# Kernel optimization log

Measured on AMD Instinct MI355X. Metric: run time of the kernel, lower is better.

Reference implementation:

```python
import jax, jax.numpy as jnp
import numpy as np

N = 8192
E = 262144
EMBED = 128
EDGE_DIM = 16
EPS = 1e-09
SLOPE = 0.01  # LeakyReLU default


def leaky_relu(x):
    return jnp.where(x >= 0, x, SLOPE * x)


def setup_inputs() -> dict:
    key = jax.random.key(0)
    ks = jax.random.split(key, 12)
    x = jax.random.randint(ks[0], (N, 1), 0, 20, dtype=jnp.int64)
    edge_index = jax.random.randint(ks[1], (2, E), 0, N, dtype=jnp.int64)
    edge_attr = jax.random.normal(ks[2], (E, EDGE_DIM), dtype=jnp.float32)
    emb = jax.random.normal(ks[3], (20, EMBED), dtype=jnp.float32)
    # conv1: nn = Linear(EMBED, 64); edge lin: EDGE_DIM -> EMBED
    W1 = jax.random.normal(ks[4], (EMBED, 64), dtype=jnp.float32) * 0.05
    b1 = jnp.zeros((64,), dtype=jnp.float32)
    E1w = jax.random.normal(ks[5], (EDGE_DIM, EMBED), dtype=jnp.float32) * 0.1
    E1b = jnp.zeros((EMBED,), dtype=jnp.float32)
    # conv6: nn = Linear(64, 32); edge lin: EDGE_DIM -> 64
    W2 = jax.random.normal(ks[6], (64, 32), dtype=jnp.float32) * 0.05
    b2 = jnp.zeros((32,), dtype=jnp.float32)
    E2w = jax.random.normal(ks[7], (EDGE_DIM, 64), dtype=jnp.float32) * 0.1
    E2b = jnp.zeros((64,), dtype=jnp.float32)
    return {"x": x, "edge_index": edge_index, "edge_attr": edge_attr,
            "emb": emb, "W1": W1, "b1": b1, "E1w": E1w, "E1b": E1b,
            "W2": W2, "b2": b2, "E2w": E2w, "E2b": E2b}


def gine_conv(h, src, dst, edge_emb, W, b):
    # message: relu(h[src] + edge_emb); aggregate: scatter-add at dst
    m = jax.nn.relu(h[src] + edge_emb)                      # [E, d]
    agg = jax.ops.segment_sum(m, dst, num_segments=N)       # [N, d]
    return ((1.0 + EPS) * h + agg) @ W + b


def reference(x, edge_index, edge_attr, emb, W1, b1, E1w, E1b, W2, b2, E2w, E2b):
    h = emb[x[:, 0]]                                         # [N, EMBED]
    src, dst = edge_index[0], edge_index[1]
    h = gine_conv(h, src, dst, edge_attr @ E1w + E1b, W1, b1)  # [N, 64]
    h = leaky_relu(h)
    h = gine_conv(h, src, dst, edge_attr @ E2w + E2b, W2, b2)  # [N, 32]
    return h @ h.T                                           # [N, N]
```

## Files before the change

### kernel.cpp

```cpp
#include <hip/hip_runtime.h>
#include <hip/hip_bf16.h>

#define NN 8192
#define NE 262144
#define EPSF 1e-9f

typedef __attribute__((ext_vector_type(8))) short short8;
typedef __attribute__((ext_vector_type(4))) float floatx4;

__global__ __launch_bounds__(256) void embed_kernel(const int* __restrict__ x,
    const float* __restrict__ emb, float* __restrict__ h0) {
  int tid = blockIdx.x * 256 + threadIdx.x;
  int n = tid >> 5, j = tid & 31;
  int xi = x[n];
  ((float4*)h0)[(size_t)n * 32 + j] = ((const float4*)emb)[xi * 32 + j];
}

__global__ __launch_bounds__(256) void degcount_kernel(const int* __restrict__ ei,
    int* __restrict__ deg) {
  int e = blockIdx.x * 256 + threadIdx.x;
  atomicAdd(&deg[ei[NE + e]], 1);
}

__global__ __launch_bounds__(256) void scan_kernel(const int* __restrict__ deg,
    int* __restrict__ rowptr, int* __restrict__ cursor) {
  __shared__ int part[256];
  int t = threadIdx.x;
  int base = t * 32;
  int local[32];
  int s = 0;
#pragma unroll
  for (int i = 0; i < 32; ++i) { local[i] = deg[base + i]; s += local[i]; }
  part[t] = s;
  __syncthreads();
  int pre = 0;
  for (int i = 0; i < t; ++i) pre += part[i];
  int run = pre;
#pragma unroll
  for (int i = 0; i < 32; ++i) {
    rowptr[base + i] = run;
    cursor[base + i] = run;
    run += local[i];
  }
  if (t == 255) rowptr[NN] = run;
}

__global__ __launch_bounds__(256) void scatter_kernel(const int* __restrict__ ei,
    int* __restrict__ cursor, int2* __restrict__ csr) {
  int e = blockIdx.x * 256 + threadIdx.x;
  int s = ei[e], d = ei[NE + e];
  int pos = atomicAdd(&cursor[d], 1);
  csr[pos] = (int2){e, s};
}

__global__ __launch_bounds__(256) void fused1_kernel(const int* __restrict__ rowptr,
    const int2* __restrict__ csr, const float* __restrict__ ea,
    const float* __restrict__ E1w, const float* __restrict__ E1b,
    const float* __restrict__ W1, const float* __restrict__ b1,
    const float* __restrict__ h0, float* __restrict__ h1) {
  __shared__ float sE[16 * 128];
  __shared__ float sEb[128];
  __shared__ float st[4][128];
  for (int i = threadIdx.x; i < 16 * 128; i += 256) sE[i] = E1w[i];
  if (threadIdx.x < 128) sEb[threadIdx.x] = E1b[threadIdx.x];
  __syncthreads();
  int lane = threadIdx.x & 63;
  int w = threadIdx.x >> 6;
  int n = blockIdx.x * 4 + w;
  int beg = rowptr[n], end = rowptr[n + 1];
  float acc0 = 0.f, acc1 = 0.f;
  int i = beg;
  for (; i + 2 <= end; i += 2) {
    int2 pa = csr[i];
    int2 pb = csr[i + 1];
    int eA = __builtin_amdgcn_readfirstlane(pa.x);
    int sA = __builtin_amdgcn_readfirstlane(pa.y);
    int eB = __builtin_amdgcn_readfirstlane(pb.x);
    int sB = __builtin_amdgcn_readfirstlane(pb.y);
    float hA0 = h0[(size_t)sA * 128 + lane];
    float hA1 = h0[(size_t)sA * 128 + lane + 64];
    float hB0 = h0[(size_t)sB * 128 + lane];
    float hB1 = h0[(size_t)sB * 128 + lane + 64];
    const float* eaA = ea + (size_t)eA * 16;
    const float* eaB = ea + (size_t)eB * 16;
    float eeA0 = sEb[lane], eeA1 = sEb[lane + 64];
    float eeB0 = sEb[lane], eeB1 = sEb[lane + 64];
#pragma unroll
    for (int k = 0; k < 16; ++k) {
      float w0 = sE[k * 128 + lane], w1 = sE[k * 128 + lane + 64];
      eeA0 += eaA[k] * w0; eeA1 += eaA[k] * w1;
      eeB0 += eaB[k] * w0; eeB1 += eaB[k] * w1;
    }
    float mA0 = hA0 + eeA0, mA1 = hA1 + eeA1;
    float mB0 = hB0 + eeB0, mB1 = hB1 + eeB1;
    acc0 += (mA0 > 0.f ? mA0 : 0.f) + (mB0 > 0.f ? mB0 : 0.f);
    acc1 += (mA1 > 0.f ? mA1 : 0.f) + (mB1 > 0.f ? mB1 : 0.f);
  }
  for (; i < end; ++i) {
    int2 p = csr[i];
    int e = __builtin_amdgcn_readfirstlane(p.x);
    int s = __builtin_amdgcn_readfirstlane(p.y);
    float h_0 = h0[(size_t)s * 128 + lane];
    float h_1 = h0[(size_t)s * 128 + lane + 64];
    const float* eav = ea + (size_t)e * 16;
    float ee0 = sEb[lane], ee1 = sEb[lane + 64];
#pragma unroll
    for (int k = 0; k < 16; ++k) {
      ee0 += eav[k] * sE[k * 128 + lane];
      ee1 += eav[k] * sE[k * 128 + lane + 64];
    }
    float m0 = h_0 + ee0, m1 = h_1 + ee1;
    acc0 += m0 > 0.f ? m0 : 0.f;
    acc1 += m1 > 0.f ? m1 : 0.f;
  }
  st[w][lane]      = (1.0f + EPSF) * h0[(size_t)n * 128 + lane] + acc0;
  st[w][lane + 64] = (1.0f + EPSF) * h0[(size_t)n * 128 + lane + 64] + acc1;
  float o = b1[lane];
#pragma unroll 16
  for (int k = 0; k < 128; ++k) o += st[w][k] * W1[k * 64 + lane];
  h1[(size_t)n * 64 + lane] = o > 0.f ? o : 0.01f * o;
}

__global__ __launch_bounds__(256) void fused2_kernel(const int* __restrict__ rowptr,
    const int2* __restrict__ csr, const float* __restrict__ ea,
    const float* __restrict__ E2w, const float* __restrict__ E2b,
    const float* __restrict__ W2, const float* __restrict__ b2,
    const float* __restrict__ h1, short* __restrict__ h2) {
  __shared__ float sE[16 * 64];
  __shared__ float sEb[64];
  __shared__ float st[4][64];
  for (int i = threadIdx.x; i < 16 * 64; i += 256) sE[i] = E2w[i];
  if (threadIdx.x < 64) sEb[threadIdx.x] = E2b[threadIdx.x];
  __syncthreads();
  int lane = threadIdx.x & 63;
  int w = threadIdx.x >> 6;
  int n = blockIdx.x * 4 + w;
  int beg = rowptr[n], end = rowptr[n + 1];
  float acc = 0.f;
  int i = beg;
  for (; i + 2 <= end; i += 2) {
    int2 pa = csr[i];
    int2 pb = csr[i + 1];
    int eA = __builtin_amdgcn_readfirstlane(pa.x);
    int sA = __builtin_amdgcn_readfirstlane(pa.y);
    int eB = __builtin_amdgcn_readfirstlane(pb.x);
    int sB = __builtin_amdgcn_readfirstlane(pb.y);
    float hA = h1[(size_t)sA * 64 + lane];
    float hB = h1[(size_t)sB * 64 + lane];
    const float* eaA = ea + (size_t)eA * 16;
    const float* eaB = ea + (size_t)eB * 16;
    float eeA = sEb[lane], eeB = sEb[lane];
#pragma unroll
    for (int k = 0; k < 16; ++k) {
      float wv = sE[k * 64 + lane];
      eeA += eaA[k] * wv;
      eeB += eaB[k] * wv;
    }
    float mA = hA + eeA, mB = hB + eeB;
    acc += (mA > 0.f ? mA : 0.f) + (mB > 0.f ? mB : 0.f);
  }
  for (; i < end; ++i) {
    int2 p = csr[i];
    int e = __builtin_amdgcn_readfirstlane(p.x);
    int s = __builtin_amdgcn_readfirstlane(p.y);
    float hv = h1[(size_t)s * 64 + lane];
    const float* eav = ea + (size_t)e * 16;
    float ee = sEb[lane];
#pragma unroll
    for (int k = 0; k < 16; ++k) ee += eav[k] * sE[k * 64 + lane];
    float m = hv + ee;
    acc += m > 0.f ? m : 0.f;
  }
  st[w][lane] = (1.0f + EPSF) * h1[(size_t)n * 64 + lane] + acc;
  int col = lane & 31;
  float o = b2[col];
#pragma unroll 16
  for (int k = 0; k < 64; ++k) o += st[w][k] * W2[k * 32 + col];
  if (lane < 32) {
    unsigned u = __builtin_bit_cast(unsigned, o);
    u += 0x7fffu + ((u >> 16) & 1u);
    h2[(size_t)n * 32 + col] = (short)(u >> 16);
  }
}

__global__ __launch_bounds__(256) void gemm_kernel(const short* __restrict__ h2,
    float* __restrict__ out) {
  int wid = (blockIdx.x * 256 + threadIdx.x) >> 6;
  int lane = threadIdx.x & 63;
  int cg = wid & 127;
  int rt = wid >> 7;
  int r = lane & 15, q = lane >> 4;
  short8 afrag = *(const short8*)(h2 + ((rt * 16 + r) * 32 + q * 8));
  floatx4 acc[4];
#pragma unroll
  for (int t = 0; t < 4; ++t) {
    short8 bfrag = *(const short8*)(h2 + ((cg * 64 + t * 16 + r) * 32 + q * 8));
    floatx4 z = {0.f, 0.f, 0.f, 0.f};
    acc[t] = __builtin_amdgcn_mfma_f32_16x16x32_bf16(afrag, bfrag, z, 0, 0, 0);
  }
  int row_base = rt * 16 + q * 4;
  int col_base = cg * 64 + r;
#pragma unroll
  for (int t = 0; t < 4; ++t)
#pragma unroll
    for (int reg = 0; reg < 4; ++reg)
      out[(size_t)(row_base + reg) * NN + col_base + t * 16] = acc[t][reg];
}

extern "C" void kernel_launch(void* const* d_in, const int* in_sizes, int n_in,
                              void* d_out, int out_size, void* d_ws, size_t ws_size,
                              hipStream_t stream) {
  const int*   x   = (const int*)d_in[0];
  const int*   ei  = (const int*)d_in[1];
  const float* ea  = (const float*)d_in[2];
  const float* emb = (const float*)d_in[3];
  const float* W1  = (const float*)d_in[4];
  const float* b1  = (const float*)d_in[5];
  const float* E1w = (const float*)d_in[6];
  const float* E1b = (const float*)d_in[7];
  const float* W2  = (const float*)d_in[8];
  const float* b2  = (const float*)d_in[9];
  const float* E2w = (const float*)d_in[10];
  const float* E2b = (const float*)d_in[11];

  float* ws     = (float*)d_ws;
  float* h0     = ws;
  float* h1     = ws + 1048576;
  short* h2     = (short*)(ws + 1572864);
  int*   deg    = (int*)(ws + 1703936);
  int*   rowptr = (int*)(ws + 1712128);
  int*   cursor = (int*)(ws + 1720832);
  int2*  csr    = (int2*)(ws + 1729024);

  hipMemsetAsync(deg, 0, NN * sizeof(int), stream);
  embed_kernel<<<1024, 256, 0, stream>>>(x, emb, h0);
  degcount_kernel<<<1024, 256, 0, stream>>>(ei, deg);
  scan_kernel<<<1, 256, 0, stream>>>(deg, rowptr, cursor);
  scatter_kernel<<<1024, 256, 0, stream>>>(ei, cursor, csr);
  fused1_kernel<<<2048, 256, 0, stream>>>(rowptr, csr, ea, E1w, E1b, W1, b1, h0, h1);
  fused2_kernel<<<2048, 256, 0, stream>>>(rowptr, csr, ea, E2w, E2b, W2, b2, h1, h2);
  gemm_kernel<<<16384, 256, 0, stream>>>(h2, (float*)d_out);
}
```

Before: 384.6 us.

## Fuse embedding lookup into conv1, unroll edge loops by four, coalesce GEMM stores

```diff
diff --git a/kernel.cpp b/kernel.cpp
--- a/kernel.cpp
+++ b/kernel.cpp
@@ -7,14 +7,6 @@
 
 typedef __attribute__((ext_vector_type(8))) short short8;
 typedef __attribute__((ext_vector_type(4))) float floatx4;
-
-__global__ __launch_bounds__(256) void embed_kernel(const int* __restrict__ x,
-    const float* __restrict__ emb, float* __restrict__ h0) {
-  int tid = blockIdx.x * 256 + threadIdx.x;
-  int n = tid >> 5, j = tid & 31;
-  int xi = x[n];
-  ((float4*)h0)[(size_t)n * 32 + j] = ((const float4*)emb)[xi * 32 + j];
-}
 
 __global__ __launch_bounds__(256) void degcount_kernel(const int* __restrict__ ei,
     int* __restrict__ deg) {
@@ -24,18 +16,25 @@
 
 __global__ __launch_bounds__(256) void scan_kernel(const int* __restrict__ deg,
     int* __restrict__ rowptr, int* __restrict__ cursor) {
-  __shared__ int part[256];
+  __shared__ int wsum[4];
   int t = threadIdx.x;
+  int lane = t & 63, w = t >> 6;
   int base = t * 32;
   int local[32];
   int s = 0;
 #pragma unroll
   for (int i = 0; i < 32; ++i) { local[i] = deg[base + i]; s += local[i]; }
-  part[t] = s;
+  int sc = s;
+#pragma unroll
+  for (int d = 1; d < 64; d <<= 1) {
+    int v = __shfl_up(sc, d);
+    if (lane >= d) sc += v;
+  }
+  if (lane == 63) wsum[w] = sc;
   __syncthreads();
-  int pre = 0;
-  for (int i = 0; i < t; ++i) pre += part[i];
-  int run = pre;
+  int woff = 0;
+  for (int u = 0; u < w; ++u) woff += wsum[u];
+  int run = woff + sc - s;
 #pragma unroll
   for (int i = 0; i < 32; ++i) {
     rowptr[base + i] = run;
@@ -57,7 +56,8 @@
     const int2* __restrict__ csr, const float* __restrict__ ea,
     const float* __restrict__ E1w, const float* __restrict__ E1b,
     const float* __restrict__ W1, const float* __restrict__ b1,
-    const float* __restrict__ h0, float* __restrict__ h1) {
+    const int* __restrict__ x, const float* __restrict__ emb,
+    float* __restrict__ h1) {
   __shared__ float sE[16 * 128];
   __shared__ float sEb[128];
   __shared__ float st[4][128];
@@ -67,41 +67,55 @@
   int lane = threadIdx.x & 63;
   int w = threadIdx.x >> 6;
   int n = blockIdx.x * 4 + w;
-  int beg = rowptr[n], end = rowptr[n + 1];
+  int beg = __builtin_amdgcn_readfirstlane(rowptr[n]);
+  int end = __builtin_amdgcn_readfirstlane(rowptr[n + 1]);
   float acc0 = 0.f, acc1 = 0.f;
   int i = beg;
-  for (; i + 2 <= end; i += 2) {
-    int2 pa = csr[i];
-    int2 pb = csr[i + 1];
-    int eA = __builtin_amdgcn_readfirstlane(pa.x);
-    int sA = __builtin_amdgcn_readfirstlane(pa.y);
-    int eB = __builtin_amdgcn_readfirstlane(pb.x);
-    int sB = __builtin_amdgcn_readfirstlane(pb.y);
-    float hA0 = h0[(size_t)sA * 128 + lane];
-    float hA1 = h0[(size_t)sA * 128 + lane + 64];
-    float hB0 = h0[(size_t)sB * 128 + lane];
-    float hB1 = h0[(size_t)sB * 128 + lane + 64];
-    const float* eaA = ea + (size_t)eA * 16;
-    const float* eaB = ea + (size_t)eB * 16;
-    float eeA0 = sEb[lane], eeA1 = sEb[lane + 64];
-    float eeB0 = sEb[lane], eeB1 = sEb[lane + 64];
+  for (; i + 4 <= end; i += 4) {
+    int2 p0 = csr[i], p1 = csr[i + 1], p2 = csr[i + 2], p3 = csr[i + 3];
+    int e0 = __builtin_amdgcn_readfirstlane(p0.x);
+    int s0 = __builtin_amdgcn_readfirstlane(p0.y);
+    int e1 = __builtin_amdgcn_readfirstlane(p1.x);
+    int s1 = __builtin_amdgcn_readfirstlane(p1.y);
+    int e2 = __builtin_amdgcn_readfirstlane(p2.x);
+    int s2 = __builtin_amdgcn_readfirstlane(p2.y);
+    int e3 = __builtin_amdgcn_readfirstlane(p3.x);
+    int s3 = __builtin_amdgcn_readfirstlane(p3.y);
+    int x0 = x[s0], x1 = x[s1], x2 = x[s2], x3 = x[s3];
+    float hA0 = emb[x0 * 128 + lane], hA1 = emb[x0 * 128 + lane + 64];
+    float hB0 = emb[x1 * 128 + lane], hB1 = emb[x1 * 128 + lane + 64];
+    float hC0 = emb[x2 * 128 + lane], hC1 = emb[x2 * 128 + lane + 64];
+    float hD0 = emb[x3 * 128 + lane], hD1 = emb[x3 * 128 + lane + 64];
+    const float* ea0 = ea + (size_t)e0 * 16;
+    const float* ea1 = ea + (size_t)e1 * 16;
+    const float* ea2 = ea + (size_t)e2 * 16;
+    const float* ea3 = ea + (size_t)e3 * 16;
+    float A0 = sEb[lane], A1 = sEb[lane + 64];
+    float B0 = A0, B1 = A1, C0 = A0, C1 = A1, D0 = A0, D1 = A1;
 #pragma unroll
     for (int k = 0; k < 16; ++k) {
       float w0 = sE[k * 128 + lane], w1 = sE[k * 128 + lane + 64];
-      eeA0 += eaA[k] * w0; eeA1 += eaA[k] * w1;
-      eeB0 += eaB[k] * w0; eeB1 += eaB[k] * w1;
+      A0 += ea0[k] * w0; A1 += ea0[k] * w1;
+      B0 += ea1[k] * w0; B1 += ea1[k] * w1;
+      C0 += ea2[k] * w0; C1 += ea2[k] * w1;
+      D0 += ea3[k] * w0; D1 += ea3[k] * w1;
     }
-    float mA0 = hA0 + eeA0, mA1 = hA1 + eeA1;
-    float mB0 = hB0 + eeB0, mB1 = hB1 + eeB1;
-    acc0 += (mA0 > 0.f ? mA0 : 0.f) + (mB0 > 0.f ? mB0 : 0.f);
-    acc1 += (mA1 > 0.f ? mA1 : 0.f) + (mB1 > 0.f ? mB1 : 0.f);
+    float mA0 = hA0 + A0, mA1 = hA1 + A1;
+    float mB0 = hB0 + B0, mB1 = hB1 + B1;
+    float mC0 = hC0 + C0, mC1 = hC1 + C1;
+    float mD0 = hD0 + D0, mD1 = hD1 + D1;
+    acc0 += (mA0 > 0.f ? mA0 : 0.f) + (mB0 > 0.f ? mB0 : 0.f)
+          + (mC0 > 0.f ? mC0 : 0.f) + (mD0 > 0.f ? mD0 : 0.f);
+    acc1 += (mA1 > 0.f ? mA1 : 0.f) + (mB1 > 0.f ? mB1 : 0.f)
+          + (mC1 > 0.f ? mC1 : 0.f) + (mD1 > 0.f ? mD1 : 0.f);
   }
   for (; i < end; ++i) {
     int2 p = csr[i];
     int e = __builtin_amdgcn_readfirstlane(p.x);
     int s = __builtin_amdgcn_readfirstlane(p.y);
-    float h_0 = h0[(size_t)s * 128 + lane];
-    float h_1 = h0[(size_t)s * 128 + lane + 64];
+    int xs = x[s];
+    float h_0 = emb[xs * 128 + lane];
+    float h_1 = emb[xs * 128 + lane + 64];
     const float* eav = ea + (size_t)e * 16;
     float ee0 = sEb[lane], ee1 = sEb[lane + 64];
 #pragma unroll
@@ -113,8 +127,9 @@
     acc0 += m0 > 0.f ? m0 : 0.f;
     acc1 += m1 > 0.f ? m1 : 0.f;
   }
-  st[w][lane]      = (1.0f + EPSF) * h0[(size_t)n * 128 + lane] + acc0;
-  st[w][lane + 64] = (1.0f + EPSF) * h0[(size_t)n * 128 + lane + 64] + acc1;
+  int xn = x[n];
+  st[w][lane]      = (1.0f + EPSF) * emb[xn * 128 + lane] + acc0;
+  st[w][lane + 64] = (1.0f + EPSF) * emb[xn * 128 + lane + 64] + acc1;
   float o = b1[lane];
 #pragma unroll 16
   for (int k = 0; k < 128; ++k) o += st[w][k] * W1[k * 64 + lane];
@@ -135,29 +150,40 @@
   int lane = threadIdx.x & 63;
   int w = threadIdx.x >> 6;
   int n = blockIdx.x * 4 + w;
-  int beg = rowptr[n], end = rowptr[n + 1];
+  int beg = __builtin_amdgcn_readfirstlane(rowptr[n]);
+  int end = __builtin_amdgcn_readfirstlane(rowptr[n + 1]);
   float acc = 0.f;
   int i = beg;
-  for (; i + 2 <= end; i += 2) {
-    int2 pa = csr[i];
-    int2 pb = csr[i + 1];
-    int eA = __builtin_amdgcn_readfirstlane(pa.x);
-    int sA = __builtin_amdgcn_readfirstlane(pa.y);
-    int eB = __builtin_amdgcn_readfirstlane(pb.x);
-    int sB = __builtin_amdgcn_readfirstlane(pb.y);
-    float hA = h1[(size_t)sA * 64 + lane];
-    float hB = h1[(size_t)sB * 64 + lane];
-    const float* eaA = ea + (size_t)eA * 16;
-    const float* eaB = ea + (size_t)eB * 16;
-    float eeA = sEb[lane], eeB = sEb[lane];
+  for (; i + 4 <= end; i += 4) {
+    int2 p0 = csr[i], p1 = csr[i + 1], p2 = csr[i + 2], p3 = csr[i + 3];
+    int e0 = __builtin_amdgcn_readfirstlane(p0.x);
+    int s0 = __builtin_amdgcn_readfirstlane(p0.y);
+    int e1 = __builtin_amdgcn_readfirstlane(p1.x);
+    int s1 = __builtin_amdgcn_readfirstlane(p1.y);
+    int e2 = __builtin_amdgcn_readfirstlane(p2.x);
+    int s2 = __builtin_amdgcn_readfirstlane(p2.y);
+    int e3 = __builtin_amdgcn_readfirstlane(p3.x);
+    int s3 = __builtin_amdgcn_readfirstlane(p3.y);
+    float hA = h1[(size_t)s0 * 64 + lane];
+    float hB = h1[(size_t)s1 * 64 + lane];
+    float hC = h1[(size_t)s2 * 64 + lane];
+    float hD = h1[(size_t)s3 * 64 + lane];
+    const float* ea0 = ea + (size_t)e0 * 16;
+    const float* ea1 = ea + (size_t)e1 * 16;
+    const float* ea2 = ea + (size_t)e2 * 16;
+    const float* ea3 = ea + (size_t)e3 * 16;
+    float A = sEb[lane], B = A, C = A, D = A;
 #pragma unroll
     for (int k = 0; k < 16; ++k) {
       float wv = sE[k * 64 + lane];
-      eeA += eaA[k] * wv;
-      eeB += eaB[k] * wv;
+      A += ea0[k] * wv;
+      B += ea1[k] * wv;
+      C += ea2[k] * wv;
+      D += ea3[k] * wv;
     }
-    float mA = hA + eeA, mB = hB + eeB;
-    acc += (mA > 0.f ? mA : 0.f) + (mB > 0.f ? mB : 0.f);
+    float mA = hA + A, mB = hB + B, mC = hC + C, mD = hD + D;
+    acc += (mA > 0.f ? mA : 0.f) + (mB > 0.f ? mB : 0.f)
+         + (mC > 0.f ? mC : 0.f) + (mD > 0.f ? mD : 0.f);
   }
   for (; i < end; ++i) {
     int2 p = csr[i];
@@ -185,8 +211,10 @@
 
 __global__ __launch_bounds__(256) void gemm_kernel(const short* __restrict__ h2,
     float* __restrict__ out) {
+  __shared__ float tile[4][16 * 68];
   int wid = (blockIdx.x * 256 + threadIdx.x) >> 6;
   int lane = threadIdx.x & 63;
+  int w = threadIdx.x >> 6;
   int cg = wid & 127;
   int rt = wid >> 7;
   int r = lane & 15, q = lane >> 4;
@@ -198,13 +226,17 @@
     floatx4 z = {0.f, 0.f, 0.f, 0.f};
     acc[t] = __builtin_amdgcn_mfma_f32_16x16x32_bf16(afrag, bfrag, z, 0, 0, 0);
   }
-  int row_base = rt * 16 + q * 4;
-  int col_base = cg * 64 + r;
+  float* T = tile[w];
 #pragma unroll
   for (int t = 0; t < 4; ++t)
 #pragma unroll
     for (int reg = 0; reg < 4; ++reg)
-      out[(size_t)(row_base + reg) * NN + col_base + t * 16] = acc[t][reg];
+      T[(q * 4 + reg) * 68 + t * 16 + r] = acc[t][reg];
+#pragma unroll
+  for (int j = 0; j < 4; ++j) {
+    float4 v = *(const float4*)&T[(j * 4 + q) * 68 + r * 4];
+    *(float4*)&out[(size_t)(rt * 16 + j * 4 + q) * NN + cg * 64 + r * 4] = v;
+  }
 }
 
 extern "C" void kernel_launch(void* const* d_in, const int* in_sizes, int n_in,
@@ -224,20 +256,18 @@
   const float* E2b = (const float*)d_in[11];
 
   float* ws     = (float*)d_ws;
-  float* h0     = ws;
-  float* h1     = ws + 1048576;
-  short* h2     = (short*)(ws + 1572864);
-  int*   deg    = (int*)(ws + 1703936);
-  int*   rowptr = (int*)(ws + 1712128);
-  int*   cursor = (int*)(ws + 1720832);
-  int2*  csr    = (int2*)(ws + 1729024);
+  float* h1     = ws;
+  short* h2     = (short*)(ws + 524288);
+  int*   deg    = (int*)(ws + 589824);
+  int*   rowptr = (int*)(ws + 598016);
+  int*   cursor = (int*)(ws + 606720);
+  int2*  csr    = (int2*)(ws + 614912);
 
   hipMemsetAsync(deg, 0, NN * sizeof(int), stream);
-  embed_kernel<<<1024, 256, 0, stream>>>(x, emb, h0);
   degcount_kernel<<<1024, 256, 0, stream>>>(ei, deg);
   scan_kernel<<<1, 256, 0, stream>>>(deg, rowptr, cursor);
   scatter_kernel<<<1024, 256, 0, stream>>>(ei, cursor, csr);
-  fused1_kernel<<<2048, 256, 0, stream>>>(rowptr, csr, ea, E1w, E1b, W1, b1, h0, h1);
+  fused1_kernel<<<2048, 256, 0, stream>>>(rowptr, csr, ea, E1w, E1b, W1, b1, x, emb, h1);
   fused2_kernel<<<2048, 256, 0, stream>>>(rowptr, csr, ea, E2w, E2b, W2, b2, h1, h2);
   gemm_kernel<<<16384, 256, 0, stream>>>(h2, (float*)d_out);
 }
```

Result: slower. 412.0 us (+7.1%).

## Fuse embed with degree count, warp-scan prefix sum, prefetch CSR pairs

Applied to the files above, without the earlier changes.

```diff
diff --git a/kernel.cpp b/kernel.cpp
--- a/kernel.cpp
+++ b/kernel.cpp
@@ -8,34 +8,37 @@
 typedef __attribute__((ext_vector_type(8))) short short8;
 typedef __attribute__((ext_vector_type(4))) float floatx4;
 
-__global__ __launch_bounds__(256) void embed_kernel(const int* __restrict__ x,
-    const float* __restrict__ emb, float* __restrict__ h0) {
+__global__ __launch_bounds__(256) void embed_deg_kernel(const int* __restrict__ x,
+    const float* __restrict__ emb, float* __restrict__ h0,
+    const int* __restrict__ ei, int* __restrict__ deg) {
   int tid = blockIdx.x * 256 + threadIdx.x;
   int n = tid >> 5, j = tid & 31;
   int xi = x[n];
   ((float4*)h0)[(size_t)n * 32 + j] = ((const float4*)emb)[xi * 32 + j];
-}
-
-__global__ __launch_bounds__(256) void degcount_kernel(const int* __restrict__ ei,
-    int* __restrict__ deg) {
-  int e = blockIdx.x * 256 + threadIdx.x;
-  atomicAdd(&deg[ei[NE + e]], 1);
+  atomicAdd(&deg[ei[NE + tid]], 1);
 }
 
 __global__ __launch_bounds__(256) void scan_kernel(const int* __restrict__ deg,
     int* __restrict__ rowptr, int* __restrict__ cursor) {
-  __shared__ int part[256];
+  __shared__ int wsum[4];
   int t = threadIdx.x;
+  int lane = t & 63, w = t >> 6;
   int base = t * 32;
   int local[32];
   int s = 0;
 #pragma unroll
   for (int i = 0; i < 32; ++i) { local[i] = deg[base + i]; s += local[i]; }
-  part[t] = s;
+  int sc = s;
+#pragma unroll
+  for (int d = 1; d < 64; d <<= 1) {
+    int v = __shfl_up(sc, d);
+    if (lane >= d) sc += v;
+  }
+  if (lane == 63) wsum[w] = sc;
   __syncthreads();
-  int pre = 0;
-  for (int i = 0; i < t; ++i) pre += part[i];
-  int run = pre;
+  int woff = 0;
+  for (int u = 0; u < w; ++u) woff += wsum[u];
+  int run = woff + sc - s;
 #pragma unroll
   for (int i = 0; i < 32; ++i) {
     rowptr[base + i] = run;
@@ -70,9 +73,10 @@
   int beg = rowptr[n], end = rowptr[n + 1];
   float acc0 = 0.f, acc1 = 0.f;
   int i = beg;
-  for (; i + 2 <= end; i += 2) {
-    int2 pa = csr[i];
-    int2 pb = csr[i + 1];
+  int2 pa, pb;
+  bool have = (i + 2 <= end);
+  if (have) { pa = csr[i]; pb = csr[i + 1]; }
+  while (have) {
     int eA = __builtin_amdgcn_readfirstlane(pa.x);
     int sA = __builtin_amdgcn_readfirstlane(pa.y);
     int eB = __builtin_amdgcn_readfirstlane(pb.x);
@@ -81,10 +85,13 @@
     float hA1 = h0[(size_t)sA * 128 + lane + 64];
     float hB0 = h0[(size_t)sB * 128 + lane];
     float hB1 = h0[(size_t)sB * 128 + lane + 64];
+    i += 2;
+    have = (i + 2 <= end);
+    if (have) { pa = csr[i]; pb = csr[i + 1]; }
     const float* eaA = ea + (size_t)eA * 16;
     const float* eaB = ea + (size_t)eB * 16;
     float eeA0 = sEb[lane], eeA1 = sEb[lane + 64];
-    float eeB0 = sEb[lane], eeB1 = sEb[lane + 64];
+    float eeB0 = eeA0, eeB1 = eeA1;
 #pragma unroll
     for (int k = 0; k < 16; ++k) {
       float w0 = sE[k * 128 + lane], w1 = sE[k * 128 + lane + 64];
@@ -138,18 +145,22 @@
   int beg = rowptr[n], end = rowptr[n + 1];
   float acc = 0.f;
   int i = beg;
-  for (; i + 2 <= end; i += 2) {
-    int2 pa = csr[i];
-    int2 pb = csr[i + 1];
+  int2 pa, pb;
+  bool have = (i + 2 <= end);
+  if (have) { pa = csr[i]; pb = csr[i + 1]; }
+  while (have) {
     int eA = __builtin_amdgcn_readfirstlane(pa.x);
     int sA = __builtin_amdgcn_readfirstlane(pa.y);
     int eB = __builtin_amdgcn_readfirstlane(pb.x);
     int sB = __builtin_amdgcn_readfirstlane(pb.y);
     float hA = h1[(size_t)sA * 64 + lane];
     float hB = h1[(size_t)sB * 64 + lane];
+    i += 2;
+    have = (i + 2 <= end);
+    if (have) { pa = csr[i]; pb = csr[i + 1]; }
     const float* eaA = ea + (size_t)eA * 16;
     const float* eaB = ea + (size_t)eB * 16;
-    float eeA = sEb[lane], eeB = sEb[lane];
+    float eeA = sEb[lane], eeB = eeA;
 #pragma unroll
     for (int k = 0; k < 16; ++k) {
       float wv = sE[k * 64 + lane];
@@ -233,8 +244,7 @@
   int2*  csr    = (int2*)(ws + 1729024);
 
   hipMemsetAsync(deg, 0, NN * sizeof(int), stream);
-  embed_kernel<<<1024, 256, 0, stream>>>(x, emb, h0);
-  degcount_kernel<<<1024, 256, 0, stream>>>(ei, deg);
+  embed_deg_kernel<<<1024, 256, 0, stream>>>(x, emb, h0, ei, deg);
   scan_kernel<<<1, 256, 0, stream>>>(deg, rowptr, cursor);
   scatter_kernel<<<1024, 256, 0, stream>>>(ei, cursor, csr);
   fused1_kernel<<<2048, 256, 0, stream>>>(rowptr, csr, ea, E1w, E1b, W1, b1, h0, h1);
```

New measurement: 380.1 us. Within noise of the previous version (-1.2%).
